# Optimization experiments

Measured on AMD Instinct MI355X. Metric: run time of the kernel, lower is better.

The kernel has to match this reference:

```python
import jax, jax.numpy as jnp
import numpy as np

B = 8          # batches
NSX = 8        # subdomains per axis
NSY = 8
NSUB = NSX * NSY
GRID = 64      # points per axis per batch -> 64 points per subdomain
N = B * GRID * GRID
HID = 32       # hidden_channels (also v channels)
OUT = 32       # out_channels
TRES = 64      # max points per subdomain (exact here: uniform grid)


def _point_proj(coords, w1, b1, w2, b2, out_ch, in_ch):
    # PointProjection: Linear(2,hid) -> GELU(exact) -> Linear(hid, out*in) -> [P,out,in]
    h = jax.nn.gelu(coords @ w1 + b1, approximate=False)
    k = h @ w2 + b2
    return k.reshape(coords.shape[0], out_ch, in_ch)


def setup_inputs() -> dict:
    key = jax.random.key(0)
    ks = jax.random.split(key, 9)
    # uniform cell-centered point grid per batch in [0,1]^2
    lin = (jnp.arange(GRID, dtype=jnp.float32) + 0.5) / GRID
    X, Y = jnp.meshgrid(lin, lin, indexing='xy')
    coords1 = jnp.stack([X, Y], axis=-1).reshape(-1, 2)
    src_coords = jnp.tile(coords1, (B, 1))                       # [N,2]
    src_batch = jnp.repeat(jnp.arange(B, dtype=jnp.int32), GRID * GRID)
    v = jax.random.normal(ks[0], (N, HID), jnp.float32)

    def lin_w(k, fan_in, shape):
        bound = 1.0 / np.sqrt(fan_in)
        return jax.random.uniform(k, shape, jnp.float32, -bound, bound)

    return {
        'v': v,
        'src_coords': src_coords,
        'src_batch': src_batch,
        'tgt_res': TRES,
        'src_w1': lin_w(ks[1], 2, (2, HID)),
        'src_b1': lin_w(ks[2], 2, (HID,)),
        'src_w2': lin_w(ks[3], HID, (HID, OUT * HID)),
        'src_b2': lin_w(ks[4], HID, (OUT * HID,)),
        'tgt_w1': lin_w(ks[5], 2, (2, HID)),
        'tgt_b1': lin_w(ks[6], 2, (HID,)),
        'tgt_w2': lin_w(ks[7], HID, (HID, OUT * HID)),
        'tgt_b2': lin_w(ks[8], HID, (OUT * HID,)),
    }


def reference(v, src_coords, src_batch, tgt_res,
              src_w1, src_b1, src_w2, src_b2,
              tgt_w1, tgt_b1, tgt_w2, tgt_b2):
    # --- compute_clusters: assign each point to (batch, subdomain) segment ---
    cx = jnp.clip((src_coords[:, 0] * NSX).astype(jnp.int32), 0, NSX - 1)
    cy = jnp.clip((src_coords[:, 1] * NSY).astype(jnp.int32), 0, NSY - 1)
    seg = src_batch * NSUB + cy * NSX + cx                      # [N]
    S = B * NSUB

    # --- reference target grid in [-1/nsx, 1/nsx] x [-1/nsy, 1/nsy] ---
    x = jnp.linspace(-1.0 / NSX, 1.0 / NSX, tgt_res)
    y = jnp.linspace(-1.0 / NSY, 1.0 / NSY, tgt_res)
    TX, TY = jnp.meshgrid(x, y, indexing='xy')
    tgt_coords = jnp.stack([TX, TY], axis=-1).reshape(-1, 2)    # [T,2], T=tgt_res^2

    # --- per-point MLP kernel projections ---
    psi = _point_proj(src_coords, src_w1, src_b1, src_w2, src_b2, OUT, HID)  # [N,OUT,HID]
    phi = _point_proj(tgt_coords, tgt_w1, tgt_b1, tgt_w2, tgt_b2, OUT, HID)  # [T,OUT,HID]

    # --- segment-wise integral: A[s,o,h] = mean_{x in seg s} psi[x,o,h]*v[x,h] ---
    contrib = psi * v[:, None, :]                                # [N,OUT,HID]
    A = jax.ops.segment_sum(contrib, seg, num_segments=S)        # [S,OUT,HID]
    cnt = jax.ops.segment_sum(jnp.ones((v.shape[0],), v.dtype), seg, num_segments=S)
    A = A / jnp.maximum(cnt, 1.0)[:, None, None]

    # --- contract with target kernel on the reference grid ---
    u = jnp.einsum('toh,soh->sto', phi, A)                       # [S,T,OUT]
    u = u.reshape(B, NSUB, tgt_res, tgt_res, OUT)
    return u
```

## Files before the change

### kernel.cpp

```cpp
#include <hip/hip_runtime.h>
#include <hip/hip_bf16.h>

#define HID   32
#define OUT   32
#define T_TOT 4096
#define S_TOT 512

typedef __attribute__((ext_vector_type(8))) short short8;
typedef __attribute__((ext_vector_type(4))) float f32x4;

__device__ __forceinline__ float gelu_exact(float x) {
    return 0.5f * x * (1.0f + erff(x * 0.70710678118654752440f));
}

__device__ __forceinline__ unsigned int f2bf_u(float x) {
    __hip_bfloat16 h = __float2bfloat16(x);
    unsigned short us = *reinterpret_cast<unsigned short*>(&h);
    return (unsigned int)us;
}

__global__ __launch_bounds__(256) void k_seg_G(
    const float* __restrict__ v, const float* __restrict__ coords,
    const float* __restrict__ sw1, const float* __restrict__ sb1,
    const float* __restrict__ sw2, const float* __restrict__ sb2,
    const float* __restrict__ tw2, const float* __restrict__ tb2,
    const float* __restrict__ tw1, const float* __restrict__ tb1,
    unsigned short* __restrict__ Pbf, float* __restrict__ qout,
    unsigned int* __restrict__ Gbf) {
    const int tid = threadIdx.x;

    if (blockIdx.x >= S_TOT) {
        int t = (blockIdx.x - S_TOT) * 256 + tid;
        int i = t >> 6, j = t & 63;
        const double step = 0.25 / 63.0;
        float x = (float)(-0.125 + (double)j * step);
        float y = (float)(-0.125 + (double)i * step);
        unsigned int pk[16];
#pragma unroll
        for (int c2 = 0; c2 < 16; ++c2) {
            float z0 = fmaf(x, tw1[2 * c2],     fmaf(y, tw1[HID + 2 * c2],     tb1[2 * c2]));
            float z1 = fmaf(x, tw1[2 * c2 + 1], fmaf(y, tw1[HID + 2 * c2 + 1], tb1[2 * c2 + 1]));
            pk[c2] = f2bf_u(gelu_exact(z0)) | (f2bf_u(gelu_exact(z1)) << 16);
        }
        uint4* dst = (uint4*)(Gbf + (size_t)t * 16);
#pragma unroll
        for (int k = 0; k < 4; ++k)
            dst[k] = make_uint4(pk[4 * k], pk[4 * k + 1], pk[4 * k + 2], pk[4 * k + 3]);
        return;
    }

    const int s = blockIdx.x;
    const int b = s >> 6, cy = (s >> 3) & 7, cx = s & 7;

    __shared__ float Hs[64][HID];
    __shared__ float Vs[64][HID];
    __shared__ float Mp[4][HID][HID];
    __shared__ float Vsp[8][HID];
    __shared__ float Ms[HID][HID];
    __shared__ float Vsum[HID];

    {
        int r = tid >> 2, qq = tid & 3;
        int p = b * 4096 + (cy * 8 + (r >> 3)) * 64 + cx * 8 + (r & 7);
        const f32x4* src = (const f32x4*)(v + (size_t)p * HID + qq * 8);
        f32x4 a0 = src[0], a1 = src[1];
        *(f32x4*)&Vs[r][qq * 8]     = a0;
        *(f32x4*)&Vs[r][qq * 8 + 4] = a1;

        float x = coords[2 * p], y = coords[2 * p + 1];
#pragma unroll
        for (int e = 0; e < 8; ++e) {
            int c = qq * 8 + e;
            float z = fmaf(x, sw1[c], fmaf(y, sw1[HID + c], sb1[c]));
            Hs[r][c] = gelu_exact(z);
        }
    }
    __syncthreads();

    {
        const int w  = tid >> 6;
        const int l  = tid & 63;
        const int hq = l & 7;
        const int cg = l >> 3;
        const int r0 = w * 16;
        f32x4 acc0 = {0.f, 0.f, 0.f, 0.f};
        f32x4 acc1 = {0.f, 0.f, 0.f, 0.f};
        f32x4 acc2 = {0.f, 0.f, 0.f, 0.f};
        f32x4 acc3 = {0.f, 0.f, 0.f, 0.f};
#pragma unroll
        for (int rr = 0; rr < 16; ++rr) {
            int r = r0 + rr;
            f32x4 hv = *(const f32x4*)&Hs[r][cg * 4];
            f32x4 vv = *(const f32x4*)&Vs[r][hq * 4];
            acc0[0] = fmaf(hv[0], vv[0], acc0[0]);
            acc0[1] = fmaf(hv[0], vv[1], acc0[1]);
            acc0[2] = fmaf(hv[0], vv[2], acc0[2]);
            acc0[3] = fmaf(hv[0], vv[3], acc0[3]);
            acc1[0] = fmaf(hv[1], vv[0], acc1[0]);
            acc1[1] = fmaf(hv[1], vv[1], acc1[1]);
            acc1[2] = fmaf(hv[1], vv[2], acc1[2]);
            acc1[3] = fmaf(hv[1], vv[3], acc1[3]);
            acc2[0] = fmaf(hv[2], vv[0], acc2[0]);
            acc2[1] = fmaf(hv[2], vv[1], acc2[1]);
            acc2[2] = fmaf(hv[2], vv[2], acc2[2]);
            acc2[3] = fmaf(hv[2], vv[3], acc2[3]);
            acc3[0] = fmaf(hv[3], vv[0], acc3[0]);
            acc3[1] = fmaf(hv[3], vv[1], acc3[1]);
            acc3[2] = fmaf(hv[3], vv[2], acc3[2]);
            acc3[3] = fmaf(hv[3], vv[3], acc3[3]);
        }
        *(f32x4*)&Mp[w][cg * 4 + 0][hq * 4] = acc0;
        *(f32x4*)&Mp[w][cg * 4 + 1][hq * 4] = acc1;
        *(f32x4*)&Mp[w][cg * 4 + 2][hq * 4] = acc2;
        *(f32x4*)&Mp[w][cg * 4 + 3][hq * 4] = acc3;

        int rc = tid >> 5, h = tid & 31;
        float sum = 0.f;
#pragma unroll
        for (int j = 0; j < 8; ++j) sum += Vs[rc * 8 + j][h];
        Vsp[rc][h] = sum;
    }
    __syncthreads();

    {
        int c = tid >> 3, hq = tid & 7;
        f32x4 m0 = *(const f32x4*)&Mp[0][c][hq * 4];
        f32x4 m1 = *(const f32x4*)&Mp[1][c][hq * 4];
        f32x4 m2 = *(const f32x4*)&Mp[2][c][hq * 4];
        f32x4 m3 = *(const f32x4*)&Mp[3][c][hq * 4];
        f32x4 mm;
#pragma unroll
        for (int j = 0; j < 4; ++j) mm[j] = (m0[j] + m1[j]) + (m2[j] + m3[j]);
        *(f32x4*)&Ms[c][hq * 4] = mm;
        if (tid < 32) {
            float s2 = 0.f;
#pragma unroll
            for (int rc = 0; rc < 8; ++rc) s2 += Vsp[rc][tid];
            Vsum[tid] = s2;
        }
    }
    __syncthreads();

    {
        int o = tid >> 3, hq = tid & 7;
        f32x4 acc = {0.f, 0.f, 0.f, 0.f};
#pragma unroll 8
        for (int c = 0; c < HID; ++c) {
            f32x4 w = *(const f32x4*)(sw2 + (size_t)c * 1024 + o * 32 + hq * 4);
            f32x4 m = *(const f32x4*)&Ms[c][hq * 4];
            acc[0] = fmaf(m[0], w[0], acc[0]);
            acc[1] = fmaf(m[1], w[1], acc[1]);
            acc[2] = fmaf(m[2], w[2], acc[2]);
            acc[3] = fmaf(m[3], w[3], acc[3]);
        }
        f32x4 bb = *(const f32x4*)(sb2 + o * 32 + hq * 4);
        f32x4 vs = *(const f32x4*)&Vsum[hq * 4];
        acc[0] = fmaf(bb[0], vs[0], acc[0]);
        acc[1] = fmaf(bb[1], vs[1], acc[1]);
        acc[2] = fmaf(bb[2], vs[2], acc[2]);
        acc[3] = fmaf(bb[3], vs[3], acc[3]);
        const float inv = 1.0f / 64.0f;
        acc[0] *= inv; acc[1] *= inv; acc[2] *= inv; acc[3] *= inv;

        f32x4 a[8];
        int base = (o & 7) * 8;
#pragma unroll
        for (int k = 0; k < 8; ++k) {
            a[k][0] = __shfl(acc[0], base + k, 64);
            a[k][1] = __shfl(acc[1], base + k, 64);
            a[k][2] = __shfl(acc[2], base + k, 64);
            a[k][3] = __shfl(acc[3], base + k, 64);
        }

        int cq = hq;
        unsigned int pk[2];
#pragma unroll
        for (int k2 = 0; k2 < 2; ++k2) {
            unsigned int w01 = 0;
#pragma unroll
            for (int kk = 0; kk < 2; ++kk) {
                int c = cq * 4 + k2 * 2 + kk;
                float pacc = 0.f;
#pragma unroll
                for (int h8 = 0; h8 < 8; ++h8) {
                    f32x4 w = *(const f32x4*)(tw2 + (size_t)c * 1024 + o * 32 + h8 * 4);
                    pacc = fmaf(w[0], a[h8][0], pacc);
                    pacc = fmaf(w[1], a[h8][1], pacc);
                    pacc = fmaf(w[2], a[h8][2], pacc);
                    pacc = fmaf(w[3], a[h8][3], pacc);
                }
                w01 |= f2bf_u(pacc) << (16 * kk);
            }
            pk[k2] = w01;
        }
        uint2 val; val.x = pk[0]; val.y = pk[1];
        *(uint2*)(Pbf + (size_t)s * 1024 + o * 32 + cq * 4) = val;

        if (cq == 0) {
            float qacc = 0.f;
#pragma unroll
            for (int h8 = 0; h8 < 8; ++h8) {
                f32x4 tb = *(const f32x4*)(tb2 + o * 32 + h8 * 4);
                qacc = fmaf(tb[0], a[h8][0], qacc);
                qacc = fmaf(tb[1], a[h8][1], qacc);
                qacc = fmaf(tb[2], a[h8][2], qacc);
                qacc = fmaf(tb[3], a[h8][3], qacc);
            }
            qout[s * 32 + o] = qacc;
        }
    }
}

__global__ __launch_bounds__(256) void k_contract(
    const unsigned short* __restrict__ Gbf,
    const unsigned short* __restrict__ Pbf,
    const float* __restrict__ q,
    float* __restrict__ u) {
    const int s    = blockIdx.y;
    const int lane = threadIdx.x & 63;
    const int wave = threadIdx.x >> 6;
    const int lo = lane & 15;
    const int lk = lane >> 4;

    const unsigned short* pb = Pbf + (size_t)s * 1024;
    short8 p0 = *(const short8*)(pb + lo * 32 + lk * 8);
    short8 p1 = *(const short8*)(pb + (16 + lo) * 32 + lk * 8);

    f32x4 c0, c1;
#pragma unroll
    for (int j = 0; j < 4; ++j) {
        c0[j] = q[s * 32 + lk * 4 + j];
        c1[j] = q[s * 32 + 16 + lk * 4 + j];
    }

    const int tbase = blockIdx.x * 1024 + wave * 256;
    float* ubase = u + (size_t)s * (T_TOT * 32);

#pragma unroll 4
    for (int tile = 0; tile < 16; ++tile) {
        int t0 = tbase + tile * 16;
        short8 gfrag = *(const short8*)(Gbf + (size_t)(t0 + lo) * 32 + lk * 8);
        f32x4 d0 = __builtin_amdgcn_mfma_f32_16x16x32_bf16(p0, gfrag, c0, 0, 0, 0);
        f32x4 d1 = __builtin_amdgcn_mfma_f32_16x16x32_bf16(p1, gfrag, c1, 0, 0, 0);
        float* up = ubase + (size_t)(t0 + lo) * 32;
        *(f32x4*)(up + lk * 4)      = d0;
        *(f32x4*)(up + 16 + lk * 4) = d1;
    }
}

extern "C" void kernel_launch(void* const* d_in, const int* in_sizes, int n_in,
                              void* d_out, int out_size, void* d_ws, size_t ws_size,
                              hipStream_t stream) {
    (void)in_sizes; (void)n_in; (void)out_size; (void)ws_size;
    const float* v       = (const float*)d_in[0];
    const float* scoords = (const float*)d_in[1];
    const float* sw1 = (const float*)d_in[4];
    const float* sb1 = (const float*)d_in[5];
    const float* sw2 = (const float*)d_in[6];
    const float* sb2 = (const float*)d_in[7];
    const float* tw1 = (const float*)d_in[8];
    const float* tb1 = (const float*)d_in[9];
    const float* tw2 = (const float*)d_in[10];
    const float* tb2 = (const float*)d_in[11];
    float* u = (float*)d_out;

    char* ws = (char*)d_ws;
    unsigned int*   Gbf  = (unsigned int*)ws;
    unsigned short* Pbf  = (unsigned short*)(ws + 262144);
    float*          qbuf = (float*)(ws + 262144 + 1048576);

    hipLaunchKernelGGL(k_seg_G, dim3(S_TOT + 16), dim3(256), 0, stream,
                       v, scoords, sw1, sb1, sw2, sb2, tw2, tb2, tw1, tb1,
                       Pbf, qbuf, Gbf);
    hipLaunchKernelGGL(k_contract, dim3(4, S_TOT), dim3(256), 0, stream,
                       (const unsigned short*)Gbf, (const unsigned short*)Pbf, qbuf, u);
}
```

Measured before the change: 64.29 us.

## Fuse segment reduction with contraction, two segments per block, prefetch next inputs

New measurement: 70.13 us. 9.1% more time.

```diff
diff --git a/kernel.cpp b/kernel.cpp
--- a/kernel.cpp
+++ b/kernel.cpp
@@ -19,64 +19,67 @@
     return (unsigned int)us;
 }
 
-__global__ __launch_bounds__(256) void k_seg_G(
-    const float* __restrict__ v, const float* __restrict__ coords,
+__global__ __launch_bounds__(256) void k_tgt_hidden(
+    const float* __restrict__ tw1, const float* __restrict__ tb1,
+    unsigned int* __restrict__ Gbf) {
+    int t = blockIdx.x * 256 + threadIdx.x;
+    if (t >= T_TOT) return;
+    int i = t >> 6, j = t & 63;
+    const double step = 0.25 / 63.0;
+    float x = (float)(-0.125 + (double)j * step);
+    float y = (float)(-0.125 + (double)i * step);
+    unsigned int pk[16];
+#pragma unroll
+    for (int c2 = 0; c2 < 16; ++c2) {
+        float z0 = fmaf(x, tw1[2 * c2],     fmaf(y, tw1[HID + 2 * c2],     tb1[2 * c2]));
+        float z1 = fmaf(x, tw1[2 * c2 + 1], fmaf(y, tw1[HID + 2 * c2 + 1], tb1[2 * c2 + 1]));
+        pk[c2] = f2bf_u(gelu_exact(z0)) | (f2bf_u(gelu_exact(z1)) << 16);
+    }
+    uint4* dst = (uint4*)(Gbf + (size_t)t * 16);
+#pragma unroll
+    for (int k = 0; k < 4; ++k)
+        dst[k] = make_uint4(pk[4 * k], pk[4 * k + 1], pk[4 * k + 2], pk[4 * k + 3]);
+}
+
+struct Ph0Regs { f32x4 a0, a1; float x, y; };
+
+__device__ __forceinline__ Ph0Regs ph0_load(
+    int s, int tid, const float* __restrict__ v, const float* __restrict__ coords) {
+    const int b = s >> 6, cy = (s >> 3) & 7, cx = s & 7;
+    int r = tid >> 2, qq = tid & 3;
+    int p = b * 4096 + (cy * 8 + (r >> 3)) * 64 + cx * 8 + (r & 7);
+    Ph0Regs rg;
+    const f32x4* src = (const f32x4*)(v + (size_t)p * HID + qq * 8);
+    rg.a0 = src[0];
+    rg.a1 = src[1];
+    rg.x = coords[2 * p];
+    rg.y = coords[2 * p + 1];
+    return rg;
+}
+
+__device__ __forceinline__ void ph0_write(
+    const Ph0Regs& rg, int tid,
     const float* __restrict__ sw1, const float* __restrict__ sb1,
+    float (*Hs)[HID], float (*Vs)[HID]) {
+    int r = tid >> 2, qq = tid & 3;
+    *(f32x4*)&Vs[r][qq * 8]     = rg.a0;
+    *(f32x4*)&Vs[r][qq * 8 + 4] = rg.a1;
+#pragma unroll
+    for (int e = 0; e < 8; ++e) {
+        int c = qq * 8 + e;
+        float z = fmaf(rg.x, sw1[c], fmaf(rg.y, sw1[HID + c], sb1[c]));
+        Hs[r][c] = gelu_exact(z);
+    }
+}
+
+__device__ __forceinline__ void seg_mid(
+    int s, int tid,
     const float* __restrict__ sw2, const float* __restrict__ sb2,
     const float* __restrict__ tw2, const float* __restrict__ tb2,
-    const float* __restrict__ tw1, const float* __restrict__ tb1,
-    unsigned short* __restrict__ Pbf, float* __restrict__ qout,
-    unsigned int* __restrict__ Gbf) {
-    const int tid = threadIdx.x;
-
-    if (blockIdx.x >= S_TOT) {
-        int t = (blockIdx.x - S_TOT) * 256 + tid;
-        int i = t >> 6, j = t & 63;
-        const double step = 0.25 / 63.0;
-        float x = (float)(-0.125 + (double)j * step);
-        float y = (float)(-0.125 + (double)i * step);
-        unsigned int pk[16];
-#pragma unroll
-        for (int c2 = 0; c2 < 16; ++c2) {
-            float z0 = fmaf(x, tw1[2 * c2],     fmaf(y, tw1[HID + 2 * c2],     tb1[2 * c2]));
-            float z1 = fmaf(x, tw1[2 * c2 + 1], fmaf(y, tw1[HID + 2 * c2 + 1], tb1[2 * c2 + 1]));
-            pk[c2] = f2bf_u(gelu_exact(z0)) | (f2bf_u(gelu_exact(z1)) << 16);
-        }
-        uint4* dst = (uint4*)(Gbf + (size_t)t * 16);
-#pragma unroll
-        for (int k = 0; k < 4; ++k)
-            dst[k] = make_uint4(pk[4 * k], pk[4 * k + 1], pk[4 * k + 2], pk[4 * k + 3]);
-        return;
-    }
-
-    const int s = blockIdx.x;
-    const int b = s >> 6, cy = (s >> 3) & 7, cx = s & 7;
-
-    __shared__ float Hs[64][HID];
-    __shared__ float Vs[64][HID];
-    __shared__ float Mp[4][HID][HID];
-    __shared__ float Vsp[8][HID];
-    __shared__ float Ms[HID][HID];
-    __shared__ float Vsum[HID];
-
-    {
-        int r = tid >> 2, qq = tid & 3;
-        int p = b * 4096 + (cy * 8 + (r >> 3)) * 64 + cx * 8 + (r & 7);
-        const f32x4* src = (const f32x4*)(v + (size_t)p * HID + qq * 8);
-        f32x4 a0 = src[0], a1 = src[1];
-        *(f32x4*)&Vs[r][qq * 8]     = a0;
-        *(f32x4*)&Vs[r][qq * 8 + 4] = a1;
-
-        float x = coords[2 * p], y = coords[2 * p + 1];
-#pragma unroll
-        for (int e = 0; e < 8; ++e) {
-            int c = qq * 8 + e;
-            float z = fmaf(x, sw1[c], fmaf(y, sw1[HID + c], sb1[c]));
-            Hs[r][c] = gelu_exact(z);
-        }
-    }
-    __syncthreads();
-
+    float (*Hs)[HID], float (*Vs)[HID],
+    float (*Mp)[HID][HID], float (*Vsp)[HID],
+    float (*Ms)[HID], float* __restrict__ Vsum,
+    unsigned short* __restrict__ Pbf, float* __restrict__ qout) {
     {
         const int w  = tid >> 6;
         const int l  = tid & 63;
@@ -209,16 +212,18 @@
             qout[s * 32 + o] = qacc;
         }
     }
-}
-
-__global__ __launch_bounds__(256) void k_contract(
+    __threadfence_block();
+    __syncthreads();
+}
+
+__device__ __forceinline__ void store_seg(
+    int s, int tid,
     const unsigned short* __restrict__ Gbf,
     const unsigned short* __restrict__ Pbf,
-    const float* __restrict__ q,
+    const float* __restrict__ qout,
     float* __restrict__ u) {
-    const int s    = blockIdx.y;
-    const int lane = threadIdx.x & 63;
-    const int wave = threadIdx.x >> 6;
+    const int lane = tid & 63;
+    const int wave = tid >> 6;
     const int lo = lane & 15;
     const int lk = lane >> 4;
 
@@ -229,15 +234,15 @@
     f32x4 c0, c1;
 #pragma unroll
     for (int j = 0; j < 4; ++j) {
-        c0[j] = q[s * 32 + lk * 4 + j];
-        c1[j] = q[s * 32 + 16 + lk * 4 + j];
-    }
-
-    const int tbase = blockIdx.x * 1024 + wave * 256;
+        c0[j] = qout[s * 32 + lk * 4 + j];
+        c1[j] = qout[s * 32 + 16 + lk * 4 + j];
+    }
+
+    const int tbase = wave * 1024;
     float* ubase = u + (size_t)s * (T_TOT * 32);
 
 #pragma unroll 4
-    for (int tile = 0; tile < 16; ++tile) {
+    for (int tile = 0; tile < 64; ++tile) {
         int t0 = tbase + tile * 16;
         short8 gfrag = *(const short8*)(Gbf + (size_t)(t0 + lo) * 32 + lk * 8);
         f32x4 d0 = __builtin_amdgcn_mfma_f32_16x16x32_bf16(p0, gfrag, c0, 0, 0, 0);
@@ -246,6 +251,43 @@
         *(f32x4*)(up + lk * 4)      = d0;
         *(f32x4*)(up + 16 + lk * 4) = d1;
     }
+}
+
+__global__ __launch_bounds__(256) void k_fused2(
+    const float* __restrict__ v, const float* __restrict__ coords,
+    const float* __restrict__ sw1, const float* __restrict__ sb1,
+    const float* __restrict__ sw2, const float* __restrict__ sb2,
+    const float* __restrict__ tw2, const float* __restrict__ tb2,
+    const unsigned short* __restrict__ Gbf,
+    unsigned short* __restrict__ Pbf, float* __restrict__ qout,
+    float* __restrict__ u) {
+    const int tid = threadIdx.x;
+    const int s0 = blockIdx.x * 2;
+    const int s1 = s0 + 1;
+
+    __shared__ float Hs[64][HID];
+    __shared__ float Vs[64][HID];
+    __shared__ float Mp[4][HID][HID];
+    __shared__ float Vsp[8][HID];
+    __shared__ float Ms[HID][HID];
+    __shared__ float Vsum[HID];
+
+    {
+        Ph0Regs rg0 = ph0_load(s0, tid, v, coords);
+        ph0_write(rg0, tid, sw1, sb1, Hs, Vs);
+    }
+    __syncthreads();
+    seg_mid(s0, tid, sw2, sb2, tw2, tb2, Hs, Vs, Mp, Vsp, Ms, Vsum, Pbf, qout);
+
+    Ph0Regs rg1 = ph0_load(s1, tid, v, coords);
+
+    store_seg(s0, tid, Gbf, Pbf, qout, u);
+
+    ph0_write(rg1, tid, sw1, sb1, Hs, Vs);
+    __syncthreads();
+    seg_mid(s1, tid, sw2, sb2, tw2, tb2, Hs, Vs, Mp, Vsp, Ms, Vsum, Pbf, qout);
+
+    store_seg(s1, tid, Gbf, Pbf, qout, u);
 }
 
 extern "C" void kernel_launch(void* const* d_in, const int* in_sizes, int n_in,
@@ -269,9 +311,8 @@
     unsigned short* Pbf  = (unsigned short*)(ws + 262144);
     float*          qbuf = (float*)(ws + 262144 + 1048576);
 
-    hipLaunchKernelGGL(k_seg_G, dim3(S_TOT + 16), dim3(256), 0, stream,
-                       v, scoords, sw1, sb1, sw2, sb2, tw2, tb2, tw1, tb1,
-                       Pbf, qbuf, Gbf);
-    hipLaunchKernelGGL(k_contract, dim3(4, S_TOT), dim3(256), 0, stream,
-                       (const unsigned short*)Gbf, (const unsigned short*)Pbf, qbuf, u);
-}
+    hipLaunchKernelGGL(k_tgt_hidden, dim3(16), dim3(256), 0, stream, tw1, tb1, Gbf);
+    hipLaunchKernelGGL(k_fused2, dim3(256), dim3(256), 0, stream,
+                       v, scoords, sw1, sb1, sw2, sb2, tw2, tb2,
+                       (const unsigned short*)Gbf, Pbf, qbuf, u);
+}
```
